# Kernel tuning notes

Hardware: AMD Instinct MI355X
Metric: run time of the kernel (lower is better)

Reference implementation:

```python
import jax, jax.numpy as jnp
import numpy as np

N_USERS = 100000
M_ITEMS = 50000
EMBED = 64
N_LAYERS = 3
NNZ = 2400000
BATCH = 8192


def setup_inputs() -> dict:
    key = jax.random.key(0)
    ks = jax.random.split(key, 8)
    user = jax.random.randint(ks[0], (BATCH,), 0, N_USERS)
    item_i = jax.random.randint(ks[1], (BATCH,), 0, M_ITEMS)
    item_j = jax.random.randint(ks[2], (BATCH,), 0, M_ITEMS)
    timestamp = jax.random.uniform(ks[3], (BATCH,), dtype=jnp.float32)
    # symmetric bipartite edge list: user->item and item->user halves
    half = NNZ // 2
    u = jax.random.randint(ks[4], (half,), 0, N_USERS)
    it = jax.random.randint(ks[5], (half,), 0, M_ITEMS) + N_USERS
    edge_src = jnp.concatenate([u, it])
    edge_dst = jnp.concatenate([it, u])
    v = jax.random.uniform(ks[6], (half,), dtype=jnp.float32)
    edge_vals = jnp.concatenate([v, v])  # symmetric normalized weights
    embed_user_0 = jax.random.normal(ks[7], (N_USERS, EMBED), dtype=jnp.float32) * 0.1
    embed_item_0 = jax.random.normal(jax.random.fold_in(key, 99), (M_ITEMS, EMBED), dtype=jnp.float32) * 0.1
    return {
        'user': user, 'item_i': item_i, 'item_j': item_j,
        'timestamp': timestamp, 'split_idx': 0,
        'edge_src': edge_src, 'edge_dst': edge_dst, 'edge_vals': edge_vals,
        'embed_user_0': embed_user_0, 'embed_item_0': embed_item_0,
    }


def reference(user, item_i, item_j, timestamp, split_idx,
              edge_src, edge_dst, edge_vals, embed_user_0, embed_item_0):
    N = N_USERS + M_ITEMS
    # LightGCN propagation: mean over layer-0..n_layers embeddings
    all_emb = jnp.concatenate([embed_user_0, embed_item_0], axis=0)  # [N, D]
    emb = all_emb
    emb_sum = all_emb
    for _ in range(N_LAYERS):
        # sparse.mm(Graph, emb): gather source features along edges, scale, segment-reduce
        emb = jax.ops.segment_sum(edge_vals[:, None] * emb[edge_dst], edge_src,
                                  num_segments=N)
        emb_sum = emb_sum + emb
    light_out = emb_sum / (N_LAYERS + 1)
    embed_user = light_out[:N_USERS]
    embed_item = light_out[N_USERS:]

    ue = embed_user[user]          # [B, D]
    ie = embed_item[item_i]        # [B, D]
    je = embed_item[item_j]        # [B, D]
    prediction_i = jnp.sum(ue * ie, axis=-1)
    prediction_j = jnp.sum(ue * je, axis=-1)

    # reg_loss uses layer-0 embeddings gathered at the batch indices
    u0 = embed_user_0[user]
    i0 = embed_item_0[item_i]
    j0 = embed_item_0[item_j]
    reg_loss = 0.5 * (jnp.sum(u0 * u0) + jnp.sum(i0 * i0) + jnp.sum(j0 * j0)) / user.shape[0]
    return prediction_i, prediction_j, reg_loss
```

## Files before the change

### kernel.cpp

```cpp
#include <hip/hip_runtime.h>

#define N_USERS 100000
#define M_ITEMS 50000
#define NNODES  (N_USERS + M_ITEMS)
#define EMBED   64
#define BATCH   8192

#define NU_E ((size_t)N_USERS * EMBED)
#define NE   ((size_t)NNODES * EMBED)

#define NPB    256
#define NBUCK  ((NNODES + NPB - 1) / NPB)
#define PBLK   256
#define HBB_N  (NBUCK * PBLK)
#define SCAN_NB ((HBB_N + 1023) / 1024)
#define PTILE  4688
#define BCAP   6784
#define PRED_BLOCKS ((BATCH * 64) / 256)

typedef unsigned int uint;

static __device__ __forceinline__ ushort f2bf(float f) {
    uint u = __float_as_uint(f);
    return (ushort)((u + 0x7fffu + ((u >> 16) & 1u)) >> 16);
}
static __device__ __forceinline__ float bf_lo(uint u) { return __uint_as_float(u << 16); }
static __device__ __forceinline__ float bf_hi(uint u) { return __uint_as_float(u & 0xffff0000u); }
static __device__ __forceinline__ float bfs(ushort u) { return __uint_as_float((uint)u << 16); }

__global__ void init_and_hist(const float* __restrict__ eu, const float* __restrict__ ei,
                              ushort* __restrict__ E0,
                              const int* __restrict__ src, int* __restrict__ Hbb,
                              int nnz, int tile) {
    __shared__ int h[NBUCK];
    if (blockIdx.x < PBLK) {
        for (int i = threadIdx.x; i < NBUCK; i += blockDim.x) h[i] = 0;
        __syncthreads();
        int base = blockIdx.x * tile;
        int end  = min(base + tile, nnz);
        for (int i = base + threadIdx.x; i < end; i += blockDim.x)
            atomicAdd(&h[src[i] >> 8], 1);
        __syncthreads();
        for (int i = threadIdx.x; i < NBUCK; i += blockDim.x)
            Hbb[i * PBLK + blockIdx.x] = h[i];
    } else {
        size_t t = (size_t)(blockIdx.x - PBLK) * blockDim.x + threadIdx.x;
        const size_t nu4 = NU_E / 4;
        const size_t n4  = NE / 4;
        if (t >= n4) return;
        float4 v = (t < nu4) ? ((const float4*)eu)[t] : ((const float4*)ei)[t - nu4];
        ((ushort4*)E0)[t] = make_ushort4(f2bf(v.x), f2bf(v.y), f2bf(v.z), f2bf(v.w));
    }
}

__global__ void scan_local(int* __restrict__ h, int* __restrict__ bsum, int n) {
    __shared__ int lds[256];
    const int tid = threadIdx.x;
    const int base = blockIdx.x * 1024 + tid * 4;
    int v[4]; int s = 0;
    #pragma unroll
    for (int c = 0; c < 4; ++c) { v[c] = (base + c < n) ? h[base + c] : 0; s += v[c]; }
    lds[tid] = s;
    __syncthreads();
    for (int off = 1; off < 256; off <<= 1) {
        int t = (tid >= off) ? lds[tid - off] : 0;
        __syncthreads();
        lds[tid] += t;
        __syncthreads();
    }
    if (tid == 255) bsum[blockIdx.x] = lds[255];
    int run = (tid > 0) ? lds[tid - 1] : 0;
    #pragma unroll
    for (int c = 0; c < 4; ++c) {
        int t = v[c];
        if (base + c < n) h[base + c] = run;
        run += t;
    }
}

__global__ void scan_add2(int* __restrict__ h, const int* __restrict__ bsum,
                          int n, int nblk) {
    __shared__ int lds[256];
    int tid = threadIdx.x;
    if (tid < 256) lds[tid] = (tid < nblk) ? bsum[tid] : 0;
    __syncthreads();
    for (int off = 1; off < 256; off <<= 1) {
        int t = (tid >= off && tid < 256) ? lds[tid - off] : 0;
        __syncthreads();
        if (tid < 256) lds[tid] += t;
        __syncthreads();
    }
    int prefix = (blockIdx.x > 0) ? lds[blockIdx.x - 1] : 0;
    int i = blockIdx.x * 1024 + tid;
    if (i < n) h[i] += prefix;
}

__global__ void __launch_bounds__(1024)
partition2(const int* __restrict__ src, const int* __restrict__ dst,
           const float* __restrict__ vals, const int* __restrict__ Hbb,
           int2* __restrict__ ebuf, int nnz, int tile) {
    __shared__ int2 data[PTILE];
    __shared__ int  cnt[NBUCK];
    __shared__ int  cur[NBUCK];
    __shared__ int  gcur[NBUCK];
    __shared__ int  s[1024];
    const int blk = blockIdx.x;
    const int tid = threadIdx.x;
    const int base = blk * tile;
    const int end  = min(base + tile, nnz);

    for (int i = tid; i < NBUCK; i += 1024) gcur[i] = Hbb[i * PBLK + blk];
    __syncthreads();

    for (int h0 = base; h0 < end; h0 += PTILE) {
        int h1 = min(h0 + PTILE, end);
        for (int i = tid; i < NBUCK; i += 1024) cnt[i] = 0;
        __syncthreads();
        for (int i = h0 + tid; i < h1; i += 1024)
            atomicAdd(&cnt[src[i] >> 8], 1);
        __syncthreads();
        s[tid] = (tid < NBUCK) ? cnt[tid] : 0;
        __syncthreads();
        for (int off = 1; off < 1024; off <<= 1) {
            int t = (tid >= off) ? s[tid - off] : 0;
            __syncthreads();
            s[tid] += t;
            __syncthreads();
        }
        if (tid < NBUCK) cur[tid] = (tid > 0) ? s[tid - 1] : 0;
        __syncthreads();
        for (int i = h0 + tid; i < h1; i += 1024) {
            int sv = src[i];
            int d  = dst[i];
            float v = vals[i];
            if (d >= N_USERS) d -= N_USERS;
            int p = atomicAdd(&cur[sv >> 8], 1);
            data[p] = make_int2((sv & 255) | (d << 8), __float_as_int(v));
        }
        __syncthreads();
        int grp = tid >> 4, lane16 = tid & 15;
        for (int b = grp; b < NBUCK; b += 64) {
            int lbeg = (b > 0) ? s[b - 1] : 0;
            int c  = cnt[b];
            int gb = gcur[b];
            for (int j = lane16; j < c; j += 16)
                ebuf[gb + j] = data[lbeg + j];
        }
        __syncthreads();
        if (tid < NBUCK) gcur[tid] += cnt[tid];
        __syncthreads();
    }
}

__global__ void __launch_bounds__(1024)
bucket_sort_perm(const int* __restrict__ Hbb, const int2* __restrict__ ebuf,
                 int* __restrict__ offs, int2* __restrict__ ep,
                 int* __restrict__ perm, int nnz) {
    __shared__ int2 data[BCAP];
    __shared__ int cnt[256], sc[256], cur[256], dsc[256];
    int b   = blockIdx.x;
    int tid = threadIdx.x;
    int beg = Hbb[b * PBLK];
    int end = (b + 1 < NBUCK) ? Hbb[(b + 1) * PBLK] : nnz;
    int blen = end - beg;
    if (tid < 256) cnt[tid] = 0;
    __syncthreads();
    for (int i = beg + tid; i < end; i += 1024)
        atomicAdd(&cnt[ebuf[i].x & 255], 1);
    __syncthreads();
    if (tid < 256) sc[tid] = cnt[tid];
    __syncthreads();
    for (int off = 1; off < 256; off <<= 1) {
        int t = (tid >= off && tid < 256) ? sc[tid - off] : 0;
        __syncthreads();
        if (tid < 256) sc[tid] += t;
        __syncthreads();
    }
    if (tid < 256) {
        int lbase = (tid > 0) ? sc[tid - 1] : 0;
        int node = b * NPB + tid;
        if (node < NNODES) offs[node] = beg + lbase;
        cur[tid] = lbase;
    }
    __syncthreads();
    if (blen <= BCAP) {
        for (int i = beg + tid; i < end; i += 1024) {
            int2 e = ebuf[i];
            int p = atomicAdd(&cur[e.x & 255], 1);
            data[p] = make_int2(e.x >> 8, e.y);
        }
        __syncthreads();
        for (int i = tid; i < blen; i += 1024)
            ep[beg + i] = data[i];
    } else {
        for (int i = beg + tid; i < end; i += 1024) {
            int2 e = ebuf[i];
            int p = atomicAdd(&cur[e.x & 255], 1);
            ep[beg + p] = make_int2(e.x >> 8, e.y);
        }
    }
    __syncthreads();
    if (tid < 256) sc[tid] = 0;
    __syncthreads();
    int nodeCount = min(NNODES - b * NPB, NPB);
    int bin = 0;
    if (tid < nodeCount) {
        bin = 255 - min(cnt[tid], 255);
        atomicAdd(&sc[bin], 1);
    }
    __syncthreads();
    if (tid < 256) dsc[tid] = sc[tid];
    __syncthreads();
    for (int off = 1; off < 256; off <<= 1) {
        int t = (tid >= off && tid < 256) ? dsc[tid - off] : 0;
        __syncthreads();
        if (tid < 256) dsc[tid] += t;
        __syncthreads();
    }
    if (tid < 256) cur[tid] = b * NPB + ((tid > 0) ? dsc[tid - 1] : 0);
    __syncthreads();
    if (tid < nodeCount) {
        int rank = atomicAdd(&cur[bin], 1);
        perm[rank] = b * NPB + tid;
    }
    if (b == 0 && tid == 0) offs[NNODES] = nnz;
}

__global__ void gather_E(const int* __restrict__ offs, const int2* __restrict__ ep,
                         const int* __restrict__ perm,
                         const ushort* __restrict__ Eprev, ushort* __restrict__ Enext,
                         int nnz) {
    int t = blockIdx.x * blockDim.x + threadIdx.x;
    int wave = t >> 6;
    int lane = t & 63;
    int g = lane >> 3;
    int q = lane & 7;
    int ln = wave * 8 + g;
    bool valid = ln < NNODES;
    int node = valid ? perm[ln] : 0;
    int start = valid ? offs[node] : 0;
    int deg   = valid ? offs[node + 1] - start : 0;
    bool isUser = node < N_USERS;
    const uint4* other = (const uint4*)(Eprev + (isUser ? NU_E : 0));
    int lastIdx = min(max(start + deg - 1, 0), nnz - 1);

    int md = deg;
    #pragma unroll
    for (int off = 8; off <= 32; off <<= 1) md = max(md, __shfl_xor(md, off));

    float a0=0.f,a1=0.f,a2=0.f,a3=0.f,a4=0.f,a5=0.f,a6=0.f,a7=0.f;
    for (int k = 0; k < md; k += 8) {
        int2 e[8];
        uint4 r[8];
        #pragma unroll
        for (int c = 0; c < 8; ++c) {
            int idx = (k + c < deg) ? start + k + c : lastIdx;
            e[c] = ep[idx];
            if (k + c >= deg) e[c].y = 0;
        }
        #pragma unroll
        for (int c = 0; c < 8; ++c)
            r[c] = other[(size_t)e[c].x * 8 + q];
        #pragma unroll
        for (int c = 0; c < 8; ++c) {
            float v = __int_as_float(e[c].y);
            a0 = fmaf(v, bf_lo(r[c].x), a0);  a1 = fmaf(v, bf_hi(r[c].x), a1);
            a2 = fmaf(v, bf_lo(r[c].y), a2);  a3 = fmaf(v, bf_hi(r[c].y), a3);
            a4 = fmaf(v, bf_lo(r[c].z), a4);  a5 = fmaf(v, bf_hi(r[c].z), a5);
            a6 = fmaf(v, bf_lo(r[c].w), a6);  a7 = fmaf(v, bf_hi(r[c].w), a7);
        }
    }

    if (!valid) return;
    uint4 o;
    o.x = (uint)f2bf(a0) | ((uint)f2bf(a1) << 16);
    o.y = (uint)f2bf(a2) | ((uint)f2bf(a3) << 16);
    o.z = (uint)f2bf(a4) | ((uint)f2bf(a5) << 16);
    o.w = (uint)f2bf(a6) | ((uint)f2bf(a7) << 16);
    ((uint4*)Enext)[(size_t)node * 8 + q] = o;
}

__global__ void predict_kernel(const int* __restrict__ user, const int* __restrict__ item_i,
                               const int* __restrict__ item_j,
                               const ushort* __restrict__ E0, const ushort* __restrict__ E1,
                               const ushort* __restrict__ E2, const ushort* __restrict__ E3,
                               const float* __restrict__ eu0, const float* __restrict__ ei0,
                               float* __restrict__ out, float* __restrict__ rbuf) {
    __shared__ float rpart[4];
    int t = blockIdx.x * blockDim.x + threadIdx.x;
    int b = t >> 6;
    int d = t & 63;
    int wv = threadIdx.x >> 6;
    float pi = 0.f, pj = 0.f, r = 0.f;
    if (b < BATCH) {
        size_t ru = (size_t)user[b] * EMBED + d;
        size_t ri = ((size_t)N_USERS + item_i[b]) * EMBED + d;
        size_t rj = ((size_t)N_USERS + item_j[b]) * EMBED + d;
        float ue = bfs(E0[ru]) + bfs(E1[ru]) + bfs(E2[ru]) + bfs(E3[ru]);
        float ie = bfs(E0[ri]) + bfs(E1[ri]) + bfs(E2[ri]) + bfs(E3[ri]);
        float je = bfs(E0[rj]) + bfs(E1[rj]) + bfs(E2[rj]) + bfs(E3[rj]);
        pi = ue * ie;
        pj = ue * je;
        float u0 = eu0[(size_t)user[b] * EMBED + d];
        float i0 = ei0[(size_t)item_i[b] * EMBED + d];
        float j0 = ei0[(size_t)item_j[b] * EMBED + d];
        r = u0 * u0 + i0 * i0 + j0 * j0;
    }
    #pragma unroll
    for (int off = 32; off > 0; off >>= 1) {
        pi += __shfl_down(pi, off);
        pj += __shfl_down(pj, off);
        r  += __shfl_down(r,  off);
    }
    if (d == 0 && b < BATCH) {
        out[b]         = pi * (1.0f / 16.0f);
        out[BATCH + b] = pj * (1.0f / 16.0f);
        rpart[wv] = r;
    }
    __syncthreads();
    if (threadIdx.x == 0)
        rbuf[blockIdx.x] = rpart[0] + rpart[1] + rpart[2] + rpart[3];
}

__global__ void finalize_reg(const float* __restrict__ rbuf, float* __restrict__ out) {
    __shared__ float lds[4];
    int tid = threadIdx.x;
    float s = 0.f;
    for (int i = tid; i < PRED_BLOCKS; i += 256) s += rbuf[i];
    #pragma unroll
    for (int off = 32; off > 0; off >>= 1) s += __shfl_down(s, off);
    if ((tid & 63) == 0) lds[tid >> 6] = s;
    __syncthreads();
    if (tid == 0)
        out[2 * BATCH] = (lds[0] + lds[1] + lds[2] + lds[3]) * (0.5f / (float)BATCH);
}

extern "C" void kernel_launch(void* const* d_in, const int* in_sizes, int n_in,
                              void* d_out, int out_size, void* d_ws, size_t ws_size,
                              hipStream_t stream) {
    const int*   user      = (const int*)  d_in[0];
    const int*   item_i    = (const int*)  d_in[1];
    const int*   item_j    = (const int*)  d_in[2];
    const int*   edge_src  = (const int*)  d_in[5];
    const int*   edge_dst  = (const int*)  d_in[6];
    const float* edge_vals = (const float*)d_in[7];
    const float* eu0       = (const float*)d_in[8];
    const float* ei0       = (const float*)d_in[9];
    const int    nnz       = in_sizes[5];

    float* out = (float*)d_out;

    ushort* E0   = (ushort*)d_ws;
    ushort* E1   = E0 + NE;
    ushort* E2   = E1 + NE;
    ushort* E3   = E2 + NE;
    int2*   ep   = (int2*)(E3 + NE);
    int*    offs = (int*)(ep + nnz);
    int*    Hbb  = offs + NNODES + 2;
    int*    bsum = Hbb + HBB_N;
    int*    perm = bsum + 256;
    float*  rbuf = (float*)(perm + NNODES);
    int2*   ebuf = (int2*)E1;

    const int tile = (nnz + PBLK - 1) / PBLK;
    const int initBlocks = (int)((NE / 4 + 1023) / 1024);

    init_and_hist<<<PBLK + initBlocks, 1024, 0, stream>>>(
        eu0, ei0, E0, edge_src, Hbb, nnz, tile);
    scan_local<<<SCAN_NB, 256, 0, stream>>>(Hbb, bsum, HBB_N);
    scan_add2<<<SCAN_NB, 1024, 0, stream>>>(Hbb, bsum, HBB_N, SCAN_NB);
    partition2<<<PBLK, 1024, 0, stream>>>(edge_src, edge_dst, edge_vals,
                                          Hbb, ebuf, nnz, tile);
    bucket_sort_perm<<<NBUCK, 1024, 0, stream>>>(Hbb, ebuf, offs, ep, perm, nnz);
    const int gblocks = (int)((((NNODES + 7) / 8) * 64 + 255) / 256);
    gather_E<<<gblocks, 256, 0, stream>>>(offs, ep, perm, E0, E1, nnz);
    gather_E<<<gblocks, 256, 0, stream>>>(offs, ep, perm, E1, E2, nnz);
    gather_E<<<gblocks, 256, 0, stream>>>(offs, ep, perm, E2, E3, nnz);
    predict_kernel<<<PRED_BLOCKS, 256, 0, stream>>>(
        user, item_i, item_j, E0, E1, E2, E3, eu0, ei0, out, rbuf);
    finalize_reg<<<1, 256, 0, stream>>>(rbuf, out);
}
```

Measured before the change: 320.8 us.

## Compute node offsets via global degree histogram and single-tile partition blocks

```diff
diff --git a/kernel.cpp b/kernel.cpp
--- a/kernel.cpp
+++ b/kernel.cpp
@@ -11,10 +11,12 @@
 
 #define NPB    256
 #define NBUCK  ((NNODES + NPB - 1) / NPB)
-#define PBLK   256
+#define PBLK   512
+#define PTILE  4688
 #define HBB_N  (NBUCK * PBLK)
-#define SCAN_NB ((HBB_N + 1023) / 1024)
-#define PTILE  4688
+#define QN     (HBB_N + NNODES)
+#define SCHUNK 2048
+#define SNB    ((QN + SCHUNK - 1) / SCHUNK)
 #define BCAP   6784
 #define PRED_BLOCKS ((BATCH * 64) / 256)
 
@@ -31,20 +33,23 @@
 __global__ void init_and_hist(const float* __restrict__ eu, const float* __restrict__ ei,
                               ushort* __restrict__ E0,
                               const int* __restrict__ src, int* __restrict__ Hbb,
-                              int nnz, int tile) {
+                              int* __restrict__ deg, int nnz) {
     __shared__ int h[NBUCK];
     if (blockIdx.x < PBLK) {
-        for (int i = threadIdx.x; i < NBUCK; i += blockDim.x) h[i] = 0;
-        __syncthreads();
-        int base = blockIdx.x * tile;
-        int end  = min(base + tile, nnz);
-        for (int i = base + threadIdx.x; i < end; i += blockDim.x)
-            atomicAdd(&h[src[i] >> 8], 1);
-        __syncthreads();
-        for (int i = threadIdx.x; i < NBUCK; i += blockDim.x)
+        for (int i = threadIdx.x; i < NBUCK; i += 1024) h[i] = 0;
+        __syncthreads();
+        int base = blockIdx.x * PTILE;
+        int end  = min(base + PTILE, nnz);
+        for (int i = base + threadIdx.x; i < end; i += 1024) {
+            int s = src[i];
+            atomicAdd(&h[s >> 8], 1);
+            atomicAdd(&deg[s], 1);
+        }
+        __syncthreads();
+        for (int i = threadIdx.x; i < NBUCK; i += 1024)
             Hbb[i * PBLK + blockIdx.x] = h[i];
     } else {
-        size_t t = (size_t)(blockIdx.x - PBLK) * blockDim.x + threadIdx.x;
+        size_t t = (size_t)(blockIdx.x - PBLK) * 1024 + threadIdx.x;
         const size_t nu4 = NU_E / 4;
         const size_t n4  = NE / 4;
         if (t >= n4) return;
@@ -56,10 +61,10 @@
 __global__ void scan_local(int* __restrict__ h, int* __restrict__ bsum, int n) {
     __shared__ int lds[256];
     const int tid = threadIdx.x;
-    const int base = blockIdx.x * 1024 + tid * 4;
-    int v[4]; int s = 0;
-    #pragma unroll
-    for (int c = 0; c < 4; ++c) { v[c] = (base + c < n) ? h[base + c] : 0; s += v[c]; }
+    const int base = blockIdx.x * SCHUNK + tid * 8;
+    int v[8]; int s = 0;
+    #pragma unroll
+    for (int c = 0; c < 8; ++c) { v[c] = (base + c < n) ? h[base + c] : 0; s += v[c]; }
     lds[tid] = s;
     __syncthreads();
     for (int off = 1; off < 256; off <<= 1) {
@@ -71,7 +76,7 @@
     if (tid == 255) bsum[blockIdx.x] = lds[255];
     int run = (tid > 0) ? lds[tid - 1] : 0;
     #pragma unroll
-    for (int c = 0; c < 4; ++c) {
+    for (int c = 0; c < 8; ++c) {
         int t = v[c];
         if (base + c < n) h[base + c] = run;
         run += t;
@@ -79,7 +84,7 @@
 }
 
 __global__ void scan_add2(int* __restrict__ h, const int* __restrict__ bsum,
-                          int n, int nblk) {
+                          int* __restrict__ offs, int n, int nblk, int nnz) {
     __shared__ int lds[256];
     int tid = threadIdx.x;
     if (tid < 256) lds[tid] = (tid < nblk) ? bsum[tid] : 0;
@@ -91,96 +96,79 @@
         __syncthreads();
     }
     int prefix = (blockIdx.x > 0) ? lds[blockIdx.x - 1] : 0;
-    int i = blockIdx.x * 1024 + tid;
-    if (i < n) h[i] += prefix;
+    int lim = min(blockIdx.x * SCHUNK + SCHUNK, n);
+    for (int i = blockIdx.x * SCHUNK + tid; i < lim; i += 1024) {
+        int v = h[i] + prefix;
+        h[i] = v;
+        if (i >= HBB_N) offs[i - HBB_N] = v - nnz;
+    }
+    if (blockIdx.x == 0 && tid == 0) offs[NNODES] = nnz;
 }
 
 __global__ void __launch_bounds__(1024)
 partition2(const int* __restrict__ src, const int* __restrict__ dst,
            const float* __restrict__ vals, const int* __restrict__ Hbb,
-           int2* __restrict__ ebuf, int nnz, int tile) {
+           int2* __restrict__ ebuf, int nnz) {
     __shared__ int2 data[PTILE];
     __shared__ int  cnt[NBUCK];
     __shared__ int  cur[NBUCK];
-    __shared__ int  gcur[NBUCK];
     __shared__ int  s[1024];
     const int blk = blockIdx.x;
     const int tid = threadIdx.x;
-    const int base = blk * tile;
-    const int end  = min(base + tile, nnz);
-
-    for (int i = tid; i < NBUCK; i += 1024) gcur[i] = Hbb[i * PBLK + blk];
-    __syncthreads();
-
-    for (int h0 = base; h0 < end; h0 += PTILE) {
-        int h1 = min(h0 + PTILE, end);
-        for (int i = tid; i < NBUCK; i += 1024) cnt[i] = 0;
-        __syncthreads();
-        for (int i = h0 + tid; i < h1; i += 1024)
-            atomicAdd(&cnt[src[i] >> 8], 1);
-        __syncthreads();
-        s[tid] = (tid < NBUCK) ? cnt[tid] : 0;
-        __syncthreads();
-        for (int off = 1; off < 1024; off <<= 1) {
-            int t = (tid >= off) ? s[tid - off] : 0;
-            __syncthreads();
-            s[tid] += t;
-            __syncthreads();
-        }
-        if (tid < NBUCK) cur[tid] = (tid > 0) ? s[tid - 1] : 0;
-        __syncthreads();
-        for (int i = h0 + tid; i < h1; i += 1024) {
-            int sv = src[i];
-            int d  = dst[i];
-            float v = vals[i];
-            if (d >= N_USERS) d -= N_USERS;
-            int p = atomicAdd(&cur[sv >> 8], 1);
-            data[p] = make_int2((sv & 255) | (d << 8), __float_as_int(v));
-        }
-        __syncthreads();
-        int grp = tid >> 4, lane16 = tid & 15;
-        for (int b = grp; b < NBUCK; b += 64) {
-            int lbeg = (b > 0) ? s[b - 1] : 0;
-            int c  = cnt[b];
-            int gb = gcur[b];
-            for (int j = lane16; j < c; j += 16)
-                ebuf[gb + j] = data[lbeg + j];
-        }
-        __syncthreads();
-        if (tid < NBUCK) gcur[tid] += cnt[tid];
-        __syncthreads();
+    const int base = blk * PTILE;
+    const int end  = min(base + PTILE, nnz);
+
+    for (int i = tid; i < NBUCK; i += 1024) cnt[i] = 0;
+    __syncthreads();
+    for (int i = base + tid; i < end; i += 1024)
+        atomicAdd(&cnt[src[i] >> 8], 1);
+    __syncthreads();
+    s[tid] = (tid < NBUCK) ? cnt[tid] : 0;
+    __syncthreads();
+    for (int off = 1; off < 1024; off <<= 1) {
+        int t = (tid >= off) ? s[tid - off] : 0;
+        __syncthreads();
+        s[tid] += t;
+        __syncthreads();
+    }
+    if (tid < NBUCK) cur[tid] = (tid > 0) ? s[tid - 1] : 0;
+    __syncthreads();
+    for (int i = base + tid; i < end; i += 1024) {
+        int sv = src[i];
+        int d  = dst[i];
+        float v = vals[i];
+        if (d >= N_USERS) d -= N_USERS;
+        int p = atomicAdd(&cur[sv >> 8], 1);
+        data[p] = make_int2((sv & 255) | (d << 8), __float_as_int(v));
+    }
+    __syncthreads();
+    int grp = tid >> 4, lane16 = tid & 15;
+    for (int b = grp; b < NBUCK; b += 64) {
+        int lbeg = (b > 0) ? s[b - 1] : 0;
+        int c  = cnt[b];
+        int gb = Hbb[b * PBLK + blk];
+        for (int j = lane16; j < c; j += 16)
+            ebuf[gb + j] = data[lbeg + j];
     }
 }
 
 __global__ void __launch_bounds__(1024)
 bucket_sort_perm(const int* __restrict__ Hbb, const int2* __restrict__ ebuf,
-                 int* __restrict__ offs, int2* __restrict__ ep,
+                 const int* __restrict__ offs, int2* __restrict__ ep,
                  int* __restrict__ perm, int nnz) {
     __shared__ int2 data[BCAP];
-    __shared__ int cnt[256], sc[256], cur[256], dsc[256];
+    __shared__ int cur[256], dg[256], sc[256], dsc[256];
     int b   = blockIdx.x;
     int tid = threadIdx.x;
     int beg = Hbb[b * PBLK];
     int end = (b + 1 < NBUCK) ? Hbb[(b + 1) * PBLK] : nnz;
     int blen = end - beg;
-    if (tid < 256) cnt[tid] = 0;
-    __syncthreads();
-    for (int i = beg + tid; i < end; i += 1024)
-        atomicAdd(&cnt[ebuf[i].x & 255], 1);
-    __syncthreads();
-    if (tid < 256) sc[tid] = cnt[tid];
-    __syncthreads();
-    for (int off = 1; off < 256; off <<= 1) {
-        int t = (tid >= off && tid < 256) ? sc[tid - off] : 0;
-        __syncthreads();
-        if (tid < 256) sc[tid] += t;
-        __syncthreads();
-    }
     if (tid < 256) {
-        int lbase = (tid > 0) ? sc[tid - 1] : 0;
         int node = b * NPB + tid;
-        if (node < NNODES) offs[node] = beg + lbase;
-        cur[tid] = lbase;
+        int o  = (node < NNODES) ? offs[node]     : nnz;
+        int o2 = (node < NNODES) ? offs[node + 1] : o;
+        cur[tid] = o - beg;
+        dg[tid]  = o2 - o;
     }
     __syncthreads();
     if (blen <= BCAP) {
@@ -205,7 +193,7 @@
     int nodeCount = min(NNODES - b * NPB, NPB);
     int bin = 0;
     if (tid < nodeCount) {
-        bin = 255 - min(cnt[tid], 255);
+        bin = min(dg[tid], 255);
         atomicAdd(&sc[bin], 1);
     }
     __syncthreads();
@@ -223,7 +211,6 @@
         int rank = atomicAdd(&cur[bin], 1);
         perm[rank] = b * NPB + tid;
     }
-    if (b == 0 && tid == 0) offs[NNODES] = nnz;
 }
 
 __global__ void gather_E(const int* __restrict__ offs, const int2* __restrict__ ep,
@@ -356,21 +343,23 @@
     ushort* E3   = E2 + NE;
     int2*   ep   = (int2*)(E3 + NE);
     int*    offs = (int*)(ep + nnz);
-    int*    Hbb  = offs + NNODES + 2;
-    int*    bsum = Hbb + HBB_N;
+    int*    Q    = offs + NNODES + 2;
+    int*    Hbb  = Q;
+    int*    deg  = Q + HBB_N;
+    int*    bsum = Q + QN;
     int*    perm = bsum + 256;
     float*  rbuf = (float*)(perm + NNODES);
     int2*   ebuf = (int2*)E1;
 
-    const int tile = (nnz + PBLK - 1) / PBLK;
     const int initBlocks = (int)((NE / 4 + 1023) / 1024);
 
+    hipMemsetAsync(deg, 0, NNODES * sizeof(int), stream);
     init_and_hist<<<PBLK + initBlocks, 1024, 0, stream>>>(
-        eu0, ei0, E0, edge_src, Hbb, nnz, tile);
-    scan_local<<<SCAN_NB, 256, 0, stream>>>(Hbb, bsum, HBB_N);
-    scan_add2<<<SCAN_NB, 1024, 0, stream>>>(Hbb, bsum, HBB_N, SCAN_NB);
+        eu0, ei0, E0, edge_src, Hbb, deg, nnz);
+    scan_local<<<SNB, 256, 0, stream>>>(Q, bsum, QN);
+    scan_add2<<<SNB, 1024, 0, stream>>>(Q, bsum, offs, QN, SNB, nnz);
     partition2<<<PBLK, 1024, 0, stream>>>(edge_src, edge_dst, edge_vals,
-                                          Hbb, ebuf, nnz, tile);
+                                          Hbb, ebuf, nnz);
     bucket_sort_perm<<<NBUCK, 1024, 0, stream>>>(Hbb, ebuf, offs, ep, perm, nnz);
     const int gblocks = (int)((((NNODES + 7) / 8) * 64 + 255) / 256);
     gather_E<<<gblocks, 256, 0, stream>>>(offs, ep, perm, E0, E1, nnz);
```

Result: slower. 406.8 us (+26.8%).
